# Optimization experiments

Measured on AMD Instinct MI355X. Metric: run time of the kernel, lower is better.

Reference implementation:

```python
import jax, jax.numpy as jnp
import numpy as np

N = 16384

def setup_inputs() -> dict:
    key = jax.random.key(0)
    k1, k2, k3 = jax.random.split(key, 3)
    risk_scores = jax.random.normal(k1, (N,), dtype=jnp.float32)
    survival_times = jax.random.normal(k2, (N,), dtype=jnp.float32)
    # 0/1 event indicator (1 = event observed, 0 = censored)
    events = (jax.random.uniform(k3, (N,)) < 0.5).astype(jnp.float32)
    return {"risk_scores": risk_scores, "survival_times": survival_times, "events": events}

def reference(risk_scores, survival_times, events):
    # Risk-set matrix: R[i, j] = 1 if T[j] >= T[i] (vectorized version of the
    # original O(n^2) double Python loop).
    R = (survival_times[None, :] >= survival_times[:, None]).astype(risk_scores.dtype)  # [n, n]
    exp_theta = jnp.exp(risk_scores)                # [n]
    # sum_j exp(theta_j) * R[i, j]  ->  matvec
    risk_set_sum = R @ exp_theta                    # [n]
    loss = -jnp.mean((risk_scores - jnp.log(risk_set_sum)) * events)
    return loss
```

## Files before the change

kernel.cpp:

```cpp
#include <hip/hip_runtime.h>
#include <math.h>

#define BLOCK 256
#define KB_ 16384
#define SCAN_T 1024

__global__ void surv_hist(const float* __restrict__ theta,
                          const float* __restrict__ T,
                          int* __restrict__ counts, float* __restrict__ bucketE,
                          float* __restrict__ Earr, int* __restrict__ elemB,
                          int* __restrict__ elemR, int n) {
    int i = blockIdx.x * BLOCK + threadIdx.x;
    if (i >= n) return;
    float Tg = T[i];
    float E  = expf(theta[i]);
    int b = (int)((Tg + 6.0f) * (KB_ / 12.0f));
    b = min(max(b, 0), KB_ - 1);
    int r = atomicAdd(&counts[b], 1);
    atomicAdd(&bucketE[b], E);
    Earr[i] = E; elemB[i] = b; elemR[i] = r;
}

__global__ void surv_scan(const int* __restrict__ counts,
                          const float* __restrict__ bucketE,
                          int* __restrict__ offsets, float* __restrict__ suffixE,
                          int n) {
    __shared__ int   ci[SCAN_T];
    __shared__ float ce[SCAN_T];
    const int t = threadIdx.x;
    const int chunk = KB_ / SCAN_T;
    const int base = t * chunk;
    int cs = 0; float es = 0.f;
    for (int k = 0; k < chunk; ++k) { cs += counts[base + k]; es += bucketE[base + k]; }
    ci[t] = cs; ce[t] = es;
    __syncthreads();
    for (int s = 1; s < SCAN_T; s <<= 1) {
        int   a = (t >= s)          ? ci[t - s] : 0;
        float f = (t + s < SCAN_T)  ? ce[t + s] : 0.f;
        __syncthreads();
        ci[t] += a; ce[t] += f;
        __syncthreads();
    }
    int run = ci[t] - cs;
    for (int k = 0; k < chunk; ++k) { offsets[base + k] = run; run += counts[base + k]; }
    float rs = ce[t] - es;
    for (int k = chunk - 1; k >= 0; --k) { rs += bucketE[base + k]; suffixE[base + k] = rs; }
    if (t == 0) { offsets[KB_] = n; suffixE[KB_] = 0.f; }
}

__global__ void surv_scatter(const float* __restrict__ T, const float* __restrict__ Earr,
                             const int* __restrict__ elemB, const int* __restrict__ elemR,
                             const int* __restrict__ offsets,
                             float* __restrict__ sortedT, float* __restrict__ sortedE, int n) {
    int i = blockIdx.x * BLOCK + threadIdx.x;
    if (i >= n) return;
    int b = elemB[i];
    int pos = offsets[b] + elemR[i];
    sortedT[pos] = T[i];
    sortedE[pos] = Earr[i];
}

__global__ void surv_risk(const float* __restrict__ theta, const float* __restrict__ T,
                          const float* __restrict__ events,
                          const int* __restrict__ elemB, const int* __restrict__ offsets,
                          const float* __restrict__ suffixE,
                          const float* __restrict__ sortedT, const float* __restrict__ sortedE,
                          float* __restrict__ bsum, int n) {
    __shared__ float red[BLOCK];
    const int tid = threadIdx.x;
    const int i = blockIdx.x * BLOCK + tid;
    float term = 0.f;
    if (i < n) {
        int b = elemB[i];
        float Ti = T[i];
        float risk = suffixE[b + 1];
        const int p0 = offsets[b], p1 = offsets[b + 1];
        for (int p = p0; p < p1; ++p)
            risk += (sortedT[p] >= Ti) ? sortedE[p] : 0.f;
        term = (theta[i] - logf(risk)) * events[i];
    }
    red[tid] = term;
    __syncthreads();
    for (int s = BLOCK / 2; s > 0; s >>= 1) {
        if (tid < s) red[tid] += red[tid + s];
        __syncthreads();
    }
    if (tid == 0) bsum[blockIdx.x] = red[0];
}

__global__ void surv_final(const float* __restrict__ bsum, float* __restrict__ out,
                           int nblocks, int n) {
    float v = 0.f;
    for (int b = threadIdx.x; b < nblocks; b += 64) v += bsum[b];
    for (int off = 32; off > 0; off >>= 1) v += __shfl_down(v, off, 64);
    if (threadIdx.x == 0) out[0] = -v / (float)n;
}

__global__ void surv_partial_bf(const float* __restrict__ theta, const float* __restrict__ T,
                                const float* __restrict__ events, float* __restrict__ bsum, int n) {
    __shared__ float red[BLOCK];
    const int tid = threadIdx.x;
    const int i = blockIdx.x * BLOCK + tid;
    float term = 0.f;
    if (i < n) {
        const float Ti = T[i];
        float risk = 0.f;
        for (int j = 0; j < n; ++j)
            risk += (T[j] >= Ti) ? expf(theta[j]) : 0.f;
        term = (theta[i] - logf(risk)) * events[i];
    }
    red[tid] = term;
    __syncthreads();
    for (int s = BLOCK / 2; s > 0; s >>= 1) {
        if (tid < s) red[tid] += red[tid + s];
        __syncthreads();
    }
    if (tid == 0) bsum[blockIdx.x] = red[0];
}

extern "C" void kernel_launch(void* const* d_in, const int* in_sizes, int n_in,
                              void* d_out, int out_size, void* d_ws, size_t ws_size,
                              hipStream_t stream) {
    const float* theta  = (const float*)d_in[0];
    const float* T      = (const float*)d_in[1];
    const float* events = (const float*)d_in[2];
    float* out = (float*)d_out;
    const int n = in_sizes[0];
    const int nbi = (n + BLOCK - 1) / BLOCK;

    const size_t need = ((size_t)2 * KB_ + 2 * (KB_ + 1) + 5 * (size_t)n + nbi) * 4;

    if ((size_t)ws_size < need) {
        float* bsum = (float*)d_ws;
        surv_partial_bf<<<nbi, BLOCK, 0, stream>>>(theta, T, events, bsum, n);
        surv_final<<<1, 64, 0, stream>>>(bsum, out, nbi, n);
        return;
    }

    int*   counts  = (int*)d_ws;
    float* bucketE = (float*)(counts + KB_);
    int*   offsets = (int*)(bucketE + KB_);
    float* suffixE = (float*)(offsets + KB_ + 1);
    float* sortedT = suffixE + KB_ + 1;
    float* sortedE = sortedT + n;
    float* Earr    = sortedE + n;
    int*   elemB   = (int*)(Earr + n);
    int*   elemR   = elemB + n;
    float* bsum    = (float*)(elemR + n);

    hipMemsetAsync(d_ws, 0, (size_t)2 * KB_ * 4, stream);
    surv_hist<<<nbi, BLOCK, 0, stream>>>(theta, T, counts, bucketE, Earr, elemB, elemR, n);
    surv_scan<<<1, SCAN_T, 0, stream>>>(counts, bucketE, offsets, suffixE, n);
    surv_scatter<<<nbi, BLOCK, 0, stream>>>(T, Earr, elemB, elemR, offsets, sortedT, sortedE, n);
    surv_risk<<<nbi, BLOCK, 0, stream>>>(theta, T, events, elemB, offsets, suffixE,
                                         sortedT, sortedE, bsum, n);
    surv_final<<<1, 64, 0, stream>>>(bsum, out, nbi, n);
}
```

Before: 81.22 us.

## Fuse scan with scatter, fold final reduction into risk kernel, shrink bucket count

Merges the bucket scan and the scatter into one single-block kernel that keeps counts in shared memory. The final reduction moves into the risk kernel using an atomic accumulator and a last-block-done counter, so two launches disappear. Bucket count drops from 16384 to 4096, which shrinks the scan but makes each bucket larger for the per-element inner loop. The fast path now requires n to be exactly 16384, and the float atomic accumulation order becomes nondeterministic.

```diff
diff --git a/kernel.cpp b/kernel.cpp
--- a/kernel.cpp
+++ b/kernel.cpp
@@ -2,77 +2,96 @@
 #include <math.h>
 
 #define BLOCK 256
-#define KB_ 16384
+#define NB 4096
 #define SCAN_T 1024
+#define EPT (16384 / SCAN_T)
 
 __global__ void surv_hist(const float* __restrict__ theta,
                           const float* __restrict__ T,
                           int* __restrict__ counts, float* __restrict__ bucketE,
                           float* __restrict__ Earr, int* __restrict__ elemB,
                           int* __restrict__ elemR, int n) {
-    int i = blockIdx.x * BLOCK + threadIdx.x;
+    const int i = blockIdx.x * BLOCK + threadIdx.x;
     if (i >= n) return;
-    float Tg = T[i];
-    float E  = expf(theta[i]);
-    int b = (int)((Tg + 6.0f) * (KB_ / 12.0f));
-    b = min(max(b, 0), KB_ - 1);
-    int r = atomicAdd(&counts[b], 1);
+    const float Tg = T[i];
+    const float E  = expf(theta[i]);
+    int b = (int)((Tg + 6.0f) * ((float)NB / 12.0f));
+    b = min(max(b, 0), NB - 1);
+    const int r = atomicAdd(&counts[b], 1);
     atomicAdd(&bucketE[b], E);
     Earr[i] = E; elemB[i] = b; elemR[i] = r;
 }
 
-__global__ void surv_scan(const int* __restrict__ counts,
-                          const float* __restrict__ bucketE,
-                          int* __restrict__ offsets, float* __restrict__ suffixE,
-                          int n) {
+__global__ void __launch_bounds__(SCAN_T)
+surv_scan_scatter(const int* __restrict__ counts, const float* __restrict__ bucketE,
+                  const float* __restrict__ T, const float* __restrict__ Earr,
+                  const int* __restrict__ elemB, const int* __restrict__ elemR,
+                  int* __restrict__ offsets, float* __restrict__ suffixE,
+                  float* __restrict__ sortedT, float* __restrict__ sortedE, int n) {
+    __shared__ int   cnt[NB + 1];
+    __shared__ float be[NB + 1];
     __shared__ int   ci[SCAN_T];
     __shared__ float ce[SCAN_T];
     const int t = threadIdx.x;
-    const int chunk = KB_ / SCAN_T;
-    const int base = t * chunk;
+    const int CH = NB / SCAN_T;
+    const int base = t * CH;
+
     int cs = 0; float es = 0.f;
-    for (int k = 0; k < chunk; ++k) { cs += counts[base + k]; es += bucketE[base + k]; }
+#pragma unroll
+    for (int k = 0; k < CH; ++k) {
+        cnt[base + k] = counts[base + k];
+        be[base + k]  = bucketE[base + k];
+        cs += cnt[base + k]; es += be[base + k];
+    }
     ci[t] = cs; ce[t] = es;
     __syncthreads();
     for (int s = 1; s < SCAN_T; s <<= 1) {
-        int   a = (t >= s)          ? ci[t - s] : 0;
-        float f = (t + s < SCAN_T)  ? ce[t + s] : 0.f;
+        const int   a = (t >= s)          ? ci[t - s] : 0;
+        const float f = (t + s < SCAN_T)  ? ce[t + s] : 0.f;
         __syncthreads();
         ci[t] += a; ce[t] += f;
         __syncthreads();
     }
-    int run = ci[t] - cs;
-    for (int k = 0; k < chunk; ++k) { offsets[base + k] = run; run += counts[base + k]; }
-    float rs = ce[t] - es;
-    for (int k = chunk - 1; k >= 0; --k) { rs += bucketE[base + k]; suffixE[base + k] = rs; }
-    if (t == 0) { offsets[KB_] = n; suffixE[KB_] = 0.f; }
+    {
+        int run = ci[t] - cs;
+        float rs = ce[t] - es;
+#pragma unroll
+        for (int k = 0; k < CH; ++k) {
+            const int c = cnt[base + k];
+            cnt[base + k] = run; offsets[base + k] = run; run += c;
+        }
+#pragma unroll
+        for (int k = CH - 1; k >= 0; --k) {
+            rs += be[base + k];
+            suffixE[base + k] = rs;
+        }
+    }
+    if (t == 0) { offsets[NB] = n; suffixE[NB] = 0.f; }
+    __syncthreads();
+
+#pragma unroll
+    for (int k = 0; k < EPT; ++k) {
+        const int i = k * SCAN_T + t;
+        const int pos = cnt[elemB[i]] + elemR[i];
+        sortedT[pos] = T[i];
+        sortedE[pos] = Earr[i];
+    }
 }
 
-__global__ void surv_scatter(const float* __restrict__ T, const float* __restrict__ Earr,
-                             const int* __restrict__ elemB, const int* __restrict__ elemR,
-                             const int* __restrict__ offsets,
-                             float* __restrict__ sortedT, float* __restrict__ sortedE, int n) {
-    int i = blockIdx.x * BLOCK + threadIdx.x;
-    if (i >= n) return;
-    int b = elemB[i];
-    int pos = offsets[b] + elemR[i];
-    sortedT[pos] = T[i];
-    sortedE[pos] = Earr[i];
-}
-
-__global__ void surv_risk(const float* __restrict__ theta, const float* __restrict__ T,
-                          const float* __restrict__ events,
-                          const int* __restrict__ elemB, const int* __restrict__ offsets,
-                          const float* __restrict__ suffixE,
-                          const float* __restrict__ sortedT, const float* __restrict__ sortedE,
-                          float* __restrict__ bsum, int n) {
+__global__ void surv_risk_final(const float* __restrict__ theta, const float* __restrict__ T,
+                                const float* __restrict__ events,
+                                const int* __restrict__ elemB, const int* __restrict__ offsets,
+                                const float* __restrict__ suffixE,
+                                const float* __restrict__ sortedT, const float* __restrict__ sortedE,
+                                float* __restrict__ acc, int* __restrict__ done,
+                                float* __restrict__ out, int n, int nblocks) {
     __shared__ float red[BLOCK];
     const int tid = threadIdx.x;
     const int i = blockIdx.x * BLOCK + tid;
     float term = 0.f;
     if (i < n) {
-        int b = elemB[i];
-        float Ti = T[i];
+        const int b = elemB[i];
+        const float Ti = T[i];
         float risk = suffixE[b + 1];
         const int p0 = offsets[b], p1 = offsets[b + 1];
         for (int p = p0; p < p1; ++p)
@@ -85,15 +104,15 @@
         if (tid < s) red[tid] += red[tid + s];
         __syncthreads();
     }
-    if (tid == 0) bsum[blockIdx.x] = red[0];
-}
-
-__global__ void surv_final(const float* __restrict__ bsum, float* __restrict__ out,
-                           int nblocks, int n) {
-    float v = 0.f;
-    for (int b = threadIdx.x; b < nblocks; b += 64) v += bsum[b];
-    for (int off = 32; off > 0; off >>= 1) v += __shfl_down(v, off, 64);
-    if (threadIdx.x == 0) out[0] = -v / (float)n;
+    if (tid == 0) {
+        atomicAdd(acc, red[0]);
+        __threadfence();
+        const int prev = atomicAdd(done, 1);
+        if (prev == nblocks - 1) {
+            const float total = atomicAdd(acc, 0.0f);
+            out[0] = -total / (float)n;
+        }
+    }
 }
 
 __global__ void surv_partial_bf(const float* __restrict__ theta, const float* __restrict__ T,
@@ -118,6 +137,14 @@
     if (tid == 0) bsum[blockIdx.x] = red[0];
 }
 
+__global__ void surv_final_bf(const float* __restrict__ bsum, float* __restrict__ out,
+                              int nblocks, int n) {
+    float v = 0.f;
+    for (int b = threadIdx.x; b < nblocks; b += 64) v += bsum[b];
+    for (int off = 32; off > 0; off >>= 1) v += __shfl_down(v, off, 64);
+    if (threadIdx.x == 0) out[0] = -v / (float)n;
+}
+
 extern "C" void kernel_launch(void* const* d_in, const int* in_sizes, int n_in,
                               void* d_out, int out_size, void* d_ws, size_t ws_size,
                               hipStream_t stream) {
@@ -128,31 +155,32 @@
     const int n = in_sizes[0];
     const int nbi = (n + BLOCK - 1) / BLOCK;
 
-    const size_t need = ((size_t)2 * KB_ + 2 * (KB_ + 1) + 5 * (size_t)n + nbi) * 4;
+    const size_t zero_words = (size_t)2 * NB + 2;
+    const size_t need = (zero_words + 2 * (NB + 1) + 5 * (size_t)n) * 4;
 
-    if ((size_t)ws_size < need) {
+    if (n != SCAN_T * EPT || ws_size < need) {
         float* bsum = (float*)d_ws;
         surv_partial_bf<<<nbi, BLOCK, 0, stream>>>(theta, T, events, bsum, n);
-        surv_final<<<1, 64, 0, stream>>>(bsum, out, nbi, n);
+        surv_final_bf<<<1, 64, 0, stream>>>(bsum, out, nbi, n);
         return;
     }
 
     int*   counts  = (int*)d_ws;
-    float* bucketE = (float*)(counts + KB_);
-    int*   offsets = (int*)(bucketE + KB_);
-    float* suffixE = (float*)(offsets + KB_ + 1);
-    float* sortedT = suffixE + KB_ + 1;
-    float* sortedE = sortedT + n;
-    float* Earr    = sortedE + n;
+    float* bucketE = (float*)(counts + NB);
+    float* acc     = bucketE + NB;
+    int*   done    = (int*)(acc + 1);
+    int*   offsets = done + 1;
+    float* suffixE = (float*)(offsets + NB + 1);
+    float* Earr    = suffixE + NB + 1;
     int*   elemB   = (int*)(Earr + n);
     int*   elemR   = elemB + n;
-    float* bsum    = (float*)(elemR + n);
+    float* sortedT = (float*)(elemR + n);
+    float* sortedE = sortedT + n;
 
-    hipMemsetAsync(d_ws, 0, (size_t)2 * KB_ * 4, stream);
+    hipMemsetAsync(d_ws, 0, zero_words * 4, stream);
     surv_hist<<<nbi, BLOCK, 0, stream>>>(theta, T, counts, bucketE, Earr, elemB, elemR, n);
-    surv_scan<<<1, SCAN_T, 0, stream>>>(counts, bucketE, offsets, suffixE, n);
-    surv_scatter<<<nbi, BLOCK, 0, stream>>>(T, Earr, elemB, elemR, offsets, sortedT, sortedE, n);
-    surv_risk<<<nbi, BLOCK, 0, stream>>>(theta, T, events, elemB, offsets, suffixE,
-                                         sortedT, sortedE, bsum, n);
-    surv_final<<<1, 64, 0, stream>>>(bsum, out, nbi, n);
+    surv_scan_scatter<<<1, SCAN_T, 0, stream>>>(counts, bucketE, T, Earr, elemB, elemR,
+                                                offsets, suffixE, sortedT, sortedE, n);
+    surv_risk_final<<<nbi, BLOCK, 0, stream>>>(theta, T, events, elemB, offsets, suffixE,
+                                               sortedT, sortedE, acc, done, out, n, nbi);
 }
```

Result: slower. 107.4 us (+32.2%).
